# Kernel optimization log

Measured on AMD Instinct MI355X. Metric: run time of the kernel, lower is better.

## Reference

```python
import jax, jax.numpy as jnp
import numpy as np

B, F, DOF, N_CLS = 256, 1024, 64, 1000

def setup_inputs() -> dict:
    key = jax.random.key(0)
    k1, k2 = jax.random.split(key)
    x = jax.random.normal(k1, (B, F), dtype=jnp.float32)
    # min/max of the input domain, as the dataloader scan would estimate on randn data
    min_x = jnp.array([-3.0], dtype=jnp.float32)
    max_x = jnp.array([3.0], dtype=jnp.float32)
    W = jax.random.normal(k2, (N_CLS, F * DOF), dtype=jnp.float32) * 0.01
    return {"x": x, "min_x": min_x, "max_x": max_x, "W": W, "dof": DOF}


def _lagrange_embed(x, min_x, max_x, dof):
    # 1D P1 Lagrange basis. simplices[t] = (t+1, t), t = 0..dof-2.
    b_, f_ = x.shape
    T = dof - 1
    h = 1.0 / T  # uniform mesh spacing on [0, 1]
    # normalize to unit interval, flatten to scalar stream of length b = B*F
    xn = ((x.reshape(-1, 1) - min_x) / (max_x - min_x)).reshape(-1)  # (b,)
    t = jnp.arange(T, dtype=xn.dtype)                                 # (T,)
    s = xn[:, None] / h                                               # (b, T) broadcastable
    lam0 = s - t            # barycentric coord of vertex t+1  (b, T)
    lam1 = (t + 1.0) - s    # barycentric coord of vertex t    (b, T)
    n2t = ((lam0 >= 0.0) & (lam1 >= 0.0)).astype(xn.dtype)            # (b, T)
    z = jnp.zeros((xn.shape[0], 1), dtype=xn.dtype)
    # mask[b, p] = number of active simplices touching vertex p (scatter of n2t to p=t and p=t+1)
    mask = jnp.concatenate([n2t, z], axis=1) + jnp.concatenate([z, n2t], axis=1)  # (b, dof)
    # shape_values[b, p] = sum over active simplices of the barycentric value at vertex p
    w0 = n2t * lam0  # goes to vertex p = t+1
    w1 = n2t * lam1  # goes to vertex p = t
    shape_vals = jnp.concatenate([w1, z], axis=1) + jnp.concatenate([z, w0], axis=1)  # (b, dof)
    basis = shape_vals / jnp.maximum(mask, 1.0)
    # rescale back to the input domain (n_features == 1, so (1,) broadcasts)
    emb = basis * (max_x - min_x) + min_x  # (b, dof)
    return emb.reshape(b_, f_ * dof)


def reference(x, min_x, max_x, W, dof):
    emb = jax.lax.stop_gradient(_lagrange_embed(x, min_x, max_x, dof))  # .detach() in torch
    return emb @ W.T  # bias-free Linear: (B, n_cls)
```

## Files before the change

kernel.cpp:

```cpp
#include <hip/hip_runtime.h>
#include <hip/hip_bf16.h>
#include <cstdint>

#define NB 256
#define NF 1024
#define NDOF 64
#define NCLS 1000
#define CTILE 128
#define FGROUP 32
#define ROWSTR 68

typedef __attribute__((ext_vector_type(8))) short short8;
typedef __attribute__((ext_vector_type(16))) float floatx16;

static __device__ inline unsigned short bfu(float f) {
    __hip_bfloat16 h = __float2bfloat16(f);
    union { __hip_bfloat16 h; unsigned short u; } cv;
    cv.h = h;
    return cv.u;
}

__global__ __launch_bounds__(256) void lagr_meta(
    const float* __restrict__ x, const float* __restrict__ mnp,
    const float* __restrict__ mxp, uint2* __restrict__ meta)
{
    __shared__ uint2 tile[32][33];
    int f0 = blockIdx.x * 32;
    int b0 = blockIdx.y * 32;
    int tid = threadIdx.x;
    float mn = mnp[0], mx = mxp[0];
    float scale = mx - mn;
    float inv = 63.0f / scale;

    int fl = tid & 31, br = tid >> 5;
#pragma unroll
    for (int i = 0; i < 4; ++i) {
        int bl = br + i * 8;
        float xv = x[(size_t)(b0 + bl) * NF + f0 + fl];
        float s = (xv - mn) * inv;
        float wA = 0.0f, wB = 0.0f;
        uint32_t t = 0u;
        if (s >= 0.0f && s <= 63.0f) {
            float tf = floorf(s);
            if (tf > 62.0f) tf = 62.0f;
            t  = (uint32_t)tf;
            wA = scale * (tf + 1.0f - s);
            wB = scale * (s - tf);
        }
        uint32_t P0 = (uint32_t)bfu(wA) | ((uint32_t)bfu(wB) << 16);
        tile[fl][bl] = make_uint2(P0, t);
    }
    __syncthreads();
    int bl = tid & 31, fr = tid >> 5;
#pragma unroll
    for (int i = 0; i < 4; ++i) {
        int f = fr + i * 8;
        meta[(size_t)(f0 + f) * NB + b0 + bl] = tile[f][bl];
    }
}

__global__ __launch_bounds__(512, 2) void lagr_main(
    const uint2* __restrict__ meta, const float* __restrict__ W,
    const float* __restrict__ mnp, float* __restrict__ out)
{
    __shared__ unsigned short wt[2][CTILE * ROWSTR];
    __shared__ float bias_s[CTILE];

    int tid  = threadIdx.x;
    int lane = tid & 63;
    int wave = tid >> 6;
    int half8 = (lane >> 5) << 3;
    int c0 = blockIdx.y * CTILE;
    int f0 = blockIdx.x * FGROUP;

    int cst = tid >> 2;
    int q4  = tid & 3;
    int crow = c0 + cst;
    if (crow > NCLS - 1) crow = NCLS - 1;
    const float* wrow = W + (size_t)crow * (NF * NDOF);

    floatx16 acc0, acc1, acc2, acc3;
#pragma unroll
    for (int r = 0; r < 16; ++r) { acc0[r] = 0.0f; acc1[r] = 0.0f; acc2[r] = 0.0f; acc3[r] = 0.0f; }
    float rowsum = 0.0f;

    float4 st[4];
    auto issue = [&](int f) {
        const float4* src = (const float4*)(wrow + ((size_t)f << 6)) + (q4 << 2);
        st[0] = src[0];
        st[1] = src[1];
        st[2] = src[2];
        st[3] = src[3];
    };
    auto commit = [&](unsigned short* buf) {
        float v[16] = { st[0].x, st[0].y, st[0].z, st[0].w,
                        st[1].x, st[1].y, st[1].z, st[1].w,
                        st[2].x, st[2].y, st[2].z, st[2].w,
                        st[3].x, st[3].y, st[3].z, st[3].w };
        uint32_t d[8];
#pragma unroll
        for (int i = 0; i < 8; ++i) {
            rowsum += v[2 * i] + v[2 * i + 1];
            d[i] = (uint32_t)bfu(v[2 * i]) | ((uint32_t)bfu(v[2 * i + 1]) << 16);
        }
        unsigned short* dst = buf + cst * ROWSTR + (q4 << 4);
        ((uint2*)dst)[0] = make_uint2(d[0], d[1]);
        ((uint2*)dst)[1] = make_uint2(d[2], d[3]);
        ((uint2*)dst)[2] = make_uint2(d[4], d[5]);
        ((uint2*)dst)[3] = make_uint2(d[6], d[7]);
    };

    unsigned short* cur = &wt[0][0];
    unsigned short* nxt = &wt[1][0];

    const uint2* mbase = meta + wave * 32 + (lane & 31);
    uint2 mcur = mbase[(size_t)f0 * NB];

    issue(f0);
    commit(cur);
    __syncthreads();

#pragma unroll 1
    for (int ch = 0; ch < FGROUP; ++ch) {
        int f = f0 + ch;
        bool more = (ch + 1 < FGROUP);
        if (more) issue(f + 1);
        uint2 mnext = mcur;
        if (more) mnext = mbase[(size_t)(f + 1) * NB];

        uint32_t P0 = mcur.x;
        uint32_t t  = mcur.y;
        uint32_t odd = t & 1u;
        uint32_t X0 = odd ? (P0 << 16) : P0;
        uint32_t X1 = odd ? (P0 >> 16) : 0u;
        int d0 = (int)(t & ~1u) - half8;

        short8 afrag[4];
#pragma unroll
        for (int kc = 0; kc < 4; ++kc) {
            union { uint32_t u[4]; short8 v; } a;
#pragma unroll
            for (int q = 0; q < 4; ++q) {
                int C = kc * 16 + 2 * q;
                a.u[q] = (d0 == C) ? X0 : (d0 == C - 2) ? X1 : 0u;
            }
            afrag[kc] = a.v;
        }

        const unsigned short* rb = cur + (lane & 31) * ROWSTR + half8;
#define CTBODY(CT, ACC) { \
        const unsigned short* r = rb + (CT) * 32 * ROWSTR; \
        _Pragma("unroll") \
        for (int kc = 0; kc < 4; ++kc) { \
            union { uint2 u2[2]; short8 v; } bf; \
            bf.u2[0] = *(const uint2*)(r + kc * 16); \
            bf.u2[1] = *(const uint2*)(r + kc * 16 + 4); \
            ACC = __builtin_amdgcn_mfma_f32_32x32x16_bf16(afrag[kc], bf.v, ACC, 0, 0, 0); \
        } }
        CTBODY(0, acc0)
        CTBODY(1, acc1)
        CTBODY(2, acc2)
        CTBODY(3, acc3)
#undef CTBODY

        if (more) commit(nxt);
        unsigned short* tmp = cur; cur = nxt; nxt = tmp;
        mcur = mnext;
        __syncthreads();
    }

    rowsum += __shfl_xor(rowsum, 1);
    rowsum += __shfl_xor(rowsum, 2);
    if (q4 == 0) bias_s[cst] = mnp[0] * rowsum;
    __syncthreads();

    int col = lane & 31;
    int rowhi = (lane >> 5) << 2;
#define EPI(CT, ACC) { \
        int c = c0 + (CT) * 32 + col; \
        if (c < NCLS) { \
            float bias = bias_s[(CT) * 32 + col]; \
            _Pragma("unroll") \
            for (int r = 0; r < 16; ++r) { \
                int brow = (r & 3) + 8 * (r >> 2) + rowhi; \
                atomicAdd(&out[(size_t)(wave * 32 + brow) * NCLS + c], ACC[r] + bias); \
            } } }
    EPI(0, acc0)
    EPI(1, acc1)
    EPI(2, acc2)
    EPI(3, acc3)
#undef EPI
}

extern "C" void kernel_launch(void* const* d_in, const int* in_sizes, int n_in,
                              void* d_out, int out_size, void* d_ws, size_t ws_size,
                              hipStream_t stream) {
    const float* x  = (const float*)d_in[0];
    const float* mn = (const float*)d_in[1];
    const float* mx = (const float*)d_in[2];
    const float* W  = (const float*)d_in[3];
    float* out = (float*)d_out;
    uint2* meta = (uint2*)d_ws;

    hipMemsetAsync(d_out, 0, (size_t)NB * NCLS * sizeof(float), stream);

    lagr_meta<<<dim3(NF / 32, NB / 32), dim3(256), 0, stream>>>(x, mn, mx, meta);

    dim3 grid(NF / FGROUP, (NCLS + CTILE - 1) / CTILE);
    lagr_main<<<grid, dim3(512), 0, stream>>>(meta, W, mn, out);
}
```

Before: 395.7 us.

## Replace atomic output accumulation with per-block partial slices plus reduction kernel

The main kernel now writes each feature-group block's results into its own partial slice in workspace instead of atomically adding into the output, and a new kernel sums the 32 slices with float4 loads. This drops the memset and the contention and serialization of atomics. In exchange it writes and rereads about 32 MB of partial data and adds a kernel launch. It also needs enough workspace for those slices.

```diff
diff --git a/kernel.cpp b/kernel.cpp
--- a/kernel.cpp
+++ b/kernel.cpp
@@ -8,6 +8,7 @@
 #define NCLS 1000
 #define CTILE 128
 #define FGROUP 32
+#define NFB (NF / FGROUP)
 #define ROWSTR 68
 
 typedef __attribute__((ext_vector_type(8))) short short8;
@@ -61,7 +62,7 @@
 
 __global__ __launch_bounds__(512, 2) void lagr_main(
     const uint2* __restrict__ meta, const float* __restrict__ W,
-    const float* __restrict__ mnp, float* __restrict__ out)
+    const float* __restrict__ mnp, float* __restrict__ part)
 {
     __shared__ unsigned short wt[2][CTILE * ROWSTR];
     __shared__ float bias_s[CTILE];
@@ -174,6 +175,7 @@
     if (q4 == 0) bias_s[cst] = mnp[0] * rowsum;
     __syncthreads();
 
+    float* pslice = part + (size_t)blockIdx.x * NB * NCLS;
     int col = lane & 31;
     int rowhi = (lane >> 5) << 2;
 #define EPI(CT, ACC) { \
@@ -183,13 +185,39 @@
             _Pragma("unroll") \
             for (int r = 0; r < 16; ++r) { \
                 int brow = (r & 3) + 8 * (r >> 2) + rowhi; \
-                atomicAdd(&out[(size_t)(wave * 32 + brow) * NCLS + c], ACC[r] + bias); \
+                pslice[(size_t)(wave * 32 + brow) * NCLS + c] = ACC[r] + bias; \
             } } }
     EPI(0, acc0)
     EPI(1, acc1)
     EPI(2, acc2)
     EPI(3, acc3)
 #undef EPI
+}
+
+__global__ __launch_bounds__(256) void lagr_reduce(
+    const float* __restrict__ part, float* __restrict__ out)
+{
+    int i = blockIdx.x * blockDim.x + threadIdx.x;
+    const float4* p = (const float4*)part;
+    float4 a0 = make_float4(0.f, 0.f, 0.f, 0.f), a1 = a0, a2 = a0, a3 = a0;
+    const int S = NB * NCLS / 4;
+#pragma unroll
+    for (int fb = 0; fb < NFB; fb += 4) {
+        float4 v0 = p[(size_t)(fb + 0) * S + i];
+        float4 v1 = p[(size_t)(fb + 1) * S + i];
+        float4 v2 = p[(size_t)(fb + 2) * S + i];
+        float4 v3 = p[(size_t)(fb + 3) * S + i];
+        a0.x += v0.x; a0.y += v0.y; a0.z += v0.z; a0.w += v0.w;
+        a1.x += v1.x; a1.y += v1.y; a1.z += v1.z; a1.w += v1.w;
+        a2.x += v2.x; a2.y += v2.y; a2.z += v2.z; a2.w += v2.w;
+        a3.x += v3.x; a3.y += v3.y; a3.z += v3.z; a3.w += v3.w;
+    }
+    float4 r;
+    r.x = (a0.x + a1.x) + (a2.x + a3.x);
+    r.y = (a0.y + a1.y) + (a2.y + a3.y);
+    r.z = (a0.z + a1.z) + (a2.z + a3.z);
+    r.w = (a0.w + a1.w) + (a2.w + a3.w);
+    ((float4*)out)[i] = r;
 }
 
 extern "C" void kernel_launch(void* const* d_in, const int* in_sizes, int n_in,
@@ -201,11 +229,12 @@
     const float* W  = (const float*)d_in[3];
     float* out = (float*)d_out;
     uint2* meta = (uint2*)d_ws;
-
-    hipMemsetAsync(d_out, 0, (size_t)NB * NCLS * sizeof(float), stream);
+    float* part = (float*)((char*)d_ws + (size_t)NF * NB * 8);
 
     lagr_meta<<<dim3(NF / 32, NB / 32), dim3(256), 0, stream>>>(x, mn, mx, meta);
 
     dim3 grid(NF / FGROUP, (NCLS + CTILE - 1) / CTILE);
-    lagr_main<<<grid, dim3(512), 0, stream>>>(meta, W, mn, out);
-}
+    lagr_main<<<grid, dim3(512), 0, stream>>>(meta, W, mn, part);
+
+    lagr_reduce<<<dim3(NB * NCLS / 4 / 256), dim3(256), 0, stream>>>(part, out);
+}
```

Result: faster. 385.2 us (-2.7%).
